# Kernel optimization log

Hardware: AMD Instinct MI355X
Metric: run time of the kernel (lower is better)

The kernel has to match this reference:

```python
import jax, jax.numpy as jnp
import numpy as np

EMBED_DIM = 256
NUM_HEADS = 8
N_Q = 300    # num queries
HW = 4096    # flattened key/value tokens
B = 16       # batch


def _linear(x, W, b):
    # torch nn.Linear: y = x @ W^T + b ; W is [out, in]
    return jnp.einsum('lbc,dc->lbd', x, W) + b


def setup_inputs() -> dict:
    key = jax.random.key(0)
    ks = jax.random.split(key, 32)
    C = EMBED_DIM
    s = 1.0 / np.sqrt(C)
    inp = {
        'query': jax.random.normal(ks[0], (N_Q, B, C), jnp.float32),
        'key': jax.random.normal(ks[1], (HW, B, C), jnp.float32),
        'value': jax.random.normal(ks[2], (HW, B, C), jnp.float32),
        'query_pos': jax.random.normal(ks[3], (N_Q, B, C), jnp.float32),
        'key_pos': jax.random.normal(ks[4], (HW, B, C), jnp.float32),
        'query_sine_embed': jax.random.normal(ks[5], (N_Q, B, C), jnp.float32),
    }
    names = ['qc', 'qp', 'qs', 'kc', 'kp', 'v', 'o']
    for i, nm in enumerate(names):
        inp[f'W_{nm}'] = jax.random.uniform(ks[6 + 2 * i], (C, C), jnp.float32, -s, s)
        inp[f'b_{nm}'] = jax.random.uniform(ks[7 + 2 * i], (C,), jnp.float32, -s, s)
    return inp


def reference(query, key, value, query_pos, key_pos, query_sine_embed,
              W_qc, b_qc, W_qp, b_qp, W_qs, b_qs, W_kc, b_kc,
              W_kp, b_kp, W_v, b_v, W_o, b_o):
    H = NUM_HEADS
    N, Bc, C = query.shape
    L = key.shape[0]
    Dh = C // H
    identity = query

    query_content = _linear(query, W_qc, b_qc)          # [N,B,C]
    key_content = _linear(key, W_kc, b_kc)              # [L,B,C]
    v = _linear(value, W_v, b_v)                        # [L,B,C]
    kp = _linear(key_pos, W_kp, b_kp)                   # [L,B,C]
    # is_first_layer == True branch
    qp = _linear(query_pos, W_qp, b_qp)                 # [N,B,C]
    q = query_content + qp
    k = key_content + kp

    qs = _linear(query_sine_embed, W_qs, b_qs)          # [N,B,C]
    # concat content and positional halves per head -> head dim 2*Dh
    q = jnp.concatenate([q.reshape(N, Bc, H, Dh), qs.reshape(N, Bc, H, Dh)], axis=3)
    k = jnp.concatenate([k.reshape(L, Bc, H, Dh), kp.reshape(L, Bc, H, Dh)], axis=3)

    q = q.transpose(1, 2, 0, 3)                          # [B,H,N,2Dh]
    k = k.transpose(1, 2, 0, 3)                          # [B,H,L,2Dh]
    v = v.reshape(L, Bc, H, Dh).transpose(1, 2, 0, 3)    # [B,H,L,Dh]

    scale = (2 * Dh) ** (-0.5)
    attn = jnp.einsum('bhnd,bhld->bhnl', q * scale, k)   # [B,H,N,L]
    attn = jax.nn.softmax(attn, axis=-1)
    out = jnp.einsum('bhnl,bhld->bhnd', attn, v)         # [B,H,N,Dh]
    out = out.transpose(0, 2, 1, 3).reshape(Bc, N, C)    # [B,N,C]
    out = jnp.einsum('bnc,dc->bnd', out, W_o) + b_o
    out = out.transpose(1, 0, 2)                         # [N,B,C]
    return identity + out
```

## Files before the change

### kernel.cpp

```cpp
#include <hip/hip_runtime.h>
#include <cstdint>
#include <cstddef>


typedef float  f4  __attribute__((ext_vector_type(4)));
typedef __bf16 b8v __attribute__((ext_vector_type(8)));

#define MFMA_BF16(a, b, c) __builtin_amdgcn_mfma_f32_16x16x32_bf16((a), (b), (c), 0, 0, 0)

#define GLD_LDS16(gp, lp)                                             \
  __builtin_amdgcn_global_load_lds(                                   \
      (const __attribute__((address_space(1))) void*)(gp),            \
      (__attribute__((address_space(3))) void*)(lp), 16, 0, 0)

__global__ __launch_bounds__(256) void convert_w(
    const float* __restrict__ W0, const float* __restrict__ W1,
    const float* __restrict__ W2, __bf16* __restrict__ Wbf)
{
  int i = blockIdx.x * 256 + threadIdx.x;
  int base = i * 4;
  int m = base >> 16;
  int off = base & 65535;
  const float* W = (m == 0) ? W0 : (m == 1) ? W1 : W2;
  float4 v = *(const float4*)(W + off);
  __bf16 o[4];
  o[0] = (__bf16)v.x; o[1] = (__bf16)v.y; o[2] = (__bf16)v.z; o[3] = (__bf16)v.w;
  *(uint2*)(Wbf + (size_t)m * 65536 + off) = *(uint2*)o;
}

__global__ __launch_bounds__(256, 2) void key_side_gemm(
    const float* __restrict__ key, const float* __restrict__ key_pos,
    const float* __restrict__ value, const __bf16* __restrict__ Wbf,
    const float* __restrict__ b_kc, const float* __restrict__ b_kp,
    const float* __restrict__ b_v,
    __bf16* __restrict__ K64, __bf16* __restrict__ V32)
{
  __shared__ char smem[65536];
  const int tid  = threadIdx.x;
  const int wave = tid >> 6, lane = tid & 63;
  const int lrow = lane & 15, quad = lane >> 4;
  const int p  = blockIdx.y;
  const int r0 = blockIdx.x * 128;
  const int rowbase = (wave & 1) * 64;
  const int colbase = (wave >> 1) * 128;

  const float* __restrict__ X = (p == 0) ? key : (p == 1) ? key_pos : value;
  const __bf16* __restrict__ Wb = Wbf + (size_t)p * 65536;
  const float* __restrict__ bias = (p == 0) ? b_kc : (p == 1) ? b_kp : b_v;

  auto stageW = [&](int buf, int kc) {
#pragma unroll
    for (int it = 0; it < 8; ++it) {
      int slot = it * 256 + tid;
      int wr = slot >> 3, gp = slot & 7;
      int g  = gp ^ (wr & 7);
      GLD_LDS16(Wb + (size_t)wr * 256 + kc + g * 8, smem + buf * 32768 + slot * 16);
    }
  };
  auto readB = [&](int buf, int ct, int kk4) -> b8v {
    int wr = colbase + ct * 16 + lrow;
    int g  = (kk4 + quad) ^ (wr & 7);
    return *(const b8v*)(smem + buf * 32768 + wr * 128 + g * 16);
  };
  auto loadA = [&](float4* x0, float4* x1, int kc) {
#pragma unroll
    for (int rt = 0; rt < 4; ++rt) {
      const float* xp = X + (size_t)(r0 + rowbase + rt * 16 + lrow) * 256 + kc + quad * 8;
      x0[rt] = *(const float4*)xp;
      x1[rt] = *(const float4*)(xp + 4);
    }
  };
  auto mk = [&](float4 x0, float4 x1) -> b8v {
    b8v t;
    t[0] = (__bf16)x0.x; t[1] = (__bf16)x0.y; t[2] = (__bf16)x0.z; t[3] = (__bf16)x0.w;
    t[4] = (__bf16)x1.x; t[5] = (__bf16)x1.y; t[6] = (__bf16)x1.z; t[7] = (__bf16)x1.w;
    return t;
  };

  f4 acc[4][8];
#pragma unroll
  for (int i = 0; i < 4; ++i)
#pragma unroll
    for (int j = 0; j < 8; ++j) acc[i][j] = f4{0.f, 0.f, 0.f, 0.f};

  float4 c0[4], c1[4], d0[4], d1[4];
  loadA(c0, c1, 0);
  stageW(0, 0);
  __syncthreads();

  for (int s = 0; s < 4; ++s) {
    const int kc0 = s * 64, buf = s & 1;
    loadA(d0, d1, kc0 + 32);
    if (s < 3) stageW(buf ^ 1, kc0 + 64);

    b8v a[4];
#pragma unroll
    for (int rt = 0; rt < 4; ++rt) a[rt] = mk(c0[rt], c1[rt]);
#pragma unroll
    for (int ct = 0; ct < 8; ++ct) {
      b8v bfr = readB(buf, ct, 0);
#pragma unroll
      for (int rt = 0; rt < 4; ++rt) acc[rt][ct] = MFMA_BF16(a[rt], bfr, acc[rt][ct]);
    }

    if (s < 3) loadA(c0, c1, kc0 + 64);

#pragma unroll
    for (int rt = 0; rt < 4; ++rt) a[rt] = mk(d0[rt], d1[rt]);
#pragma unroll
    for (int ct = 0; ct < 8; ++ct) {
      b8v bfr = readB(buf, ct, 4);
#pragma unroll
      for (int rt = 0; rt < 4; ++rt) acc[rt][ct] = MFMA_BF16(a[rt], bfr, acc[rt][ct]);
    }
    __syncthreads();
  }

  __bf16* Os = (__bf16*)smem;
#pragma unroll
  for (int ct = 0; ct < 8; ++ct) {
    int col = colbase + ct * 16 + lrow;
    float bv = bias[col];
#pragma unroll
    for (int rt = 0; rt < 4; ++rt)
#pragma unroll
      for (int r = 0; r < 4; ++r) {
        int row = rowbase + rt * 16 + quad * 4 + r;
        Os[row * 256 + col] = (__bf16)(acc[rt][ct][r] + bv);
      }
  }
  __syncthreads();
#pragma unroll
  for (int it = 0; it < 16; ++it) {
    int chunk = it * 64 + wave * 16 + (lane & 15);
    int q = lane >> 4;
    int row = chunk >> 3, h = chunk & 7;
    int R = r0 + row, l = R >> 4, bb = R & 15;
    uint4 v = *(const uint4*)(Os + chunk * 32 + q * 8);
    __bf16* dst = (p == 2) ? (V32 + ((size_t)(bb * 8 + h) * 4096 + l) * 32)
                           : (K64 + ((size_t)(bb * 8 + h) * 4096 + l) * 64 + p * 32);
    *(uint4*)(dst + q * 8) = v;
  }
}

__global__ __launch_bounds__(256) void query_side_gemm(
    const float* __restrict__ query, const float* __restrict__ query_pos,
    const float* __restrict__ query_sine,
    const float* __restrict__ W_qc, const float* __restrict__ b_qc,
    const float* __restrict__ W_qp, const float* __restrict__ b_qp,
    const float* __restrict__ W_qs, const float* __restrict__ b_qs,
    __bf16* __restrict__ Q64)
{
  __shared__ __bf16 Ws[256][72];
  const int tid  = threadIdx.x;
  const int wave = tid >> 6, lane = tid & 63;
  const int lrow = lane & 15, quad = lane >> 4;
  const int r0 = blockIdx.x * 64;

  f4 acc[16];
#pragma unroll
  for (int i = 0; i < 16; ++i) acc[i] = f4{0.f, 0.f, 0.f, 0.f};

  for (int kc = 0; kc < 768; kc += 64) {
    const float* X; const float* W;
    if (kc < 256)      { X = query;      W = W_qc; }
    else if (kc < 512) { X = query_pos;  W = W_qp; }
    else               { X = query_sine; W = W_qs; }
    const int ko = kc & 255;
#pragma unroll
    for (int it = 0; it < 16; ++it) {
      int idx = it * 256 + tid;
      int row = idx >> 4, c4 = idx & 15;
      float4 w = *(const float4*)(W + (size_t)row * 256 + ko + c4 * 4);
      __bf16* dp = &Ws[row][c4 * 4];
      dp[0] = (__bf16)w.x; dp[1] = (__bf16)w.y; dp[2] = (__bf16)w.z; dp[3] = (__bf16)w.w;
    }
    __syncthreads();
#pragma unroll
    for (int kk = 0; kk < 64; kk += 32) {
      const float* xp = X + (size_t)(r0 + wave * 16 + lrow) * 256 + ko + kk + quad * 8;
      float4 x0 = *(const float4*)xp;
      float4 x1 = *(const float4*)(xp + 4);
      b8v a;
      a[0] = (__bf16)x0.x; a[1] = (__bf16)x0.y; a[2] = (__bf16)x0.z; a[3] = (__bf16)x0.w;
      a[4] = (__bf16)x1.x; a[5] = (__bf16)x1.y; a[6] = (__bf16)x1.z; a[7] = (__bf16)x1.w;
#pragma unroll
      for (int ct = 0; ct < 16; ++ct) {
        b8v bf = *(const b8v*)&Ws[ct * 16 + lrow][kk + quad * 8];
        acc[ct] = MFMA_BF16(a, bf, acc[ct]);
      }
    }
    __syncthreads();
    if (kc == 448) {
#pragma unroll
      for (int ct = 0; ct < 16; ++ct) {
        int col = ct * 16 + lrow;
        float bsum = b_qc[col] + b_qp[col];
        int h = col >> 5, d = col & 31;
#pragma unroll
        for (int r = 0; r < 4; ++r) {
          int row = r0 + wave * 16 + quad * 4 + r;
          int n = row >> 4, bb = row & 15;
          Q64[((size_t)(bb * 8 + h) * 320 + n) * 64 + d] = (__bf16)((acc[ct][r] + bsum) * 0.125f);
        }
      }
    }
  }
#pragma unroll
  for (int ct = 0; ct < 16; ++ct) {
    int col = ct * 16 + lrow;
    float bsum = b_qc[col] + b_qp[col] + b_qs[col];
    int h = col >> 5, d = col & 31;
#pragma unroll
    for (int r = 0; r < 4; ++r) {
      int row = r0 + wave * 16 + quad * 4 + r;
      int n = row >> 4, bb = row & 15;
      Q64[((size_t)(bb * 8 + h) * 320 + n) * 64 + 32 + d] = (__bf16)((acc[ct][r] + bsum) * 0.125f);
    }
  }
}

__global__ __launch_bounds__(256) void attn_kernel(
    const __bf16* __restrict__ Q64, const __bf16* __restrict__ K64,
    const __bf16* __restrict__ V32, __bf16* __restrict__ Obf)
{
  __shared__ __bf16 Ks[128][72];
  __shared__ __bf16 Vt[32][136];
  __shared__ __bf16 Ps[64][136];
  const int tid  = threadIdx.x;
  const int wave = tid >> 6, lane = tid & 63;
  const int lrow = lane & 15, quad = lane >> 4;
  const int bh = blockIdx.y;
  const int n0 = blockIdx.x * 64;

  const __bf16* Qb = Q64 + ((size_t)bh * 320 + n0 + wave * 16 + lrow) * 64;
  const b8v qa0 = *(const b8v*)(Qb + quad * 8);
  const b8v qa1 = *(const b8v*)(Qb + 32 + quad * 8);

  const __bf16* Kb = K64 + (size_t)bh * 4096 * 64;
  const __bf16* Vb = V32 + (size_t)bh * 4096 * 32;

  float mst[4], lst[4];
#pragma unroll
  for (int i = 0; i < 4; ++i) { mst[i] = -1e30f; lst[i] = 0.f; }
  f4 oacc[2];
  oacc[0] = f4{0.f, 0.f, 0.f, 0.f};
  oacc[1] = f4{0.f, 0.f, 0.f, 0.f};

  for (int l0 = 0; l0 < 4096; l0 += 128) {
#pragma unroll
    for (int it = 0; it < 4; ++it) {
      int idx = it * 256 + tid;
      int row = idx >> 3, s = idx & 7;
      *(uint4*)&Ks[row][s * 8] = *(const uint4*)(Kb + (size_t)(l0 + row) * 64 + s * 8);
    }
#pragma unroll
    for (int it = 0; it < 2; ++it) {
      int idx = it * 256 + tid;
      int row = idx >> 2, s = idx & 3;
      uint4 u = *(const uint4*)(Vb + (size_t)(l0 + row) * 32 + s * 8);
      __bf16 tmp[8]; *(uint4*)tmp = u;
      int pc = ((row & 15) << 3) | (row >> 4);
#pragma unroll
      for (int j = 0; j < 8; ++j) Vt[s * 8 + j][pc] = tmp[j];
    }
    __syncthreads();

    f4 sc[8];
#pragma unroll
    for (int ct = 0; ct < 8; ++ct) {
      b8v kb0 = *(const b8v*)&Ks[ct * 16 + lrow][quad * 8];
      b8v kb1 = *(const b8v*)&Ks[ct * 16 + lrow][32 + quad * 8];
      f4 z = f4{0.f, 0.f, 0.f, 0.f};
      z = MFMA_BF16(qa0, kb0, z);
      z = MFMA_BF16(qa1, kb1, z);
      sc[ct] = z;
    }

    float rmax[4], rsum[4], alpha[4];
#pragma unroll
    for (int r = 0; r < 4; ++r) {
      float v = sc[0][r];
#pragma unroll
      for (int ct = 1; ct < 8; ++ct) v = fmaxf(v, sc[ct][r]);
      rmax[r] = v;
    }
#pragma unroll
    for (int off = 8; off >= 1; off >>= 1)
#pragma unroll
      for (int r = 0; r < 4; ++r)
        rmax[r] = fmaxf(rmax[r], __shfl_xor(rmax[r], off, 16));
#pragma unroll
    for (int r = 0; r < 4; ++r) {
      float mnew = fmaxf(mst[r], rmax[r]);
      alpha[r] = __expf(mst[r] - mnew);
      mst[r] = mnew;
    }
#pragma unroll
    for (int ct = 0; ct < 8; ++ct)
#pragma unroll
      for (int r = 0; r < 4; ++r)
        sc[ct][r] = __expf(sc[ct][r] - mst[r]);
#pragma unroll
    for (int r = 0; r < 4; ++r) {
      float v = sc[0][r];
#pragma unroll
      for (int ct = 1; ct < 8; ++ct) v += sc[ct][r];
      rsum[r] = v;
    }
#pragma unroll
    for (int off = 8; off >= 1; off >>= 1)
#pragma unroll
      for (int r = 0; r < 4; ++r)
        rsum[r] += __shfl_xor(rsum[r], off, 16);
#pragma unroll
    for (int r = 0; r < 4; ++r) lst[r] = lst[r] * alpha[r] + rsum[r];
#pragma unroll
    for (int c2 = 0; c2 < 2; ++c2)
#pragma unroll
      for (int r = 0; r < 4; ++r) oacc[c2][r] *= alpha[r];

#pragma unroll
    for (int r = 0; r < 4; ++r) {
      b8v pv;
#pragma unroll
      for (int ct = 0; ct < 8; ++ct) pv[ct] = (__bf16)sc[ct][r];
      *(b8v*)&Ps[wave * 16 + quad * 4 + r][lrow * 8] = pv;
    }

#pragma unroll
    for (int kt = 0; kt < 4; ++kt) {
      b8v pa = *(const b8v*)&Ps[wave * 16 + lrow][kt * 32 + quad * 8];
#pragma unroll
      for (int c2 = 0; c2 < 2; ++c2) {
        b8v vb = *(const b8v*)&Vt[c2 * 16 + lrow][kt * 32 + quad * 8];
        oacc[c2] = MFMA_BF16(pa, vb, oacc[c2]);
      }
    }
    __syncthreads();
  }

  const int bb = bh >> 3, h = bh & 7;
#pragma unroll
  for (int r = 0; r < 4; ++r) {
    int n = n0 + wave * 16 + quad * 4 + r;
    if (n < 300) {
      float inv = 1.0f / lst[r];
#pragma unroll
      for (int c2 = 0; c2 < 2; ++c2) {
        int col = h * 32 + c2 * 16 + lrow;
        Obf[((size_t)bb * 300 + n) * 256 + col] = (__bf16)(oacc[c2][r] * inv);
      }
    }
  }
}

__global__ __launch_bounds__(256) void out_proj_gemm(
    const __bf16* __restrict__ Obf, const float* __restrict__ W_o,
    const float* __restrict__ b_o, const float* __restrict__ query,
    float* __restrict__ out)
{
  __shared__ __bf16 Ws[256][72];
  const int tid  = threadIdx.x;
  const int wave = tid >> 6, lane = tid & 63;
  const int lrow = lane & 15, quad = lane >> 4;
  const int r0 = blockIdx.x * 64;

  f4 acc[16];
#pragma unroll
  for (int i = 0; i < 16; ++i) acc[i] = f4{0.f, 0.f, 0.f, 0.f};

  for (int kc0 = 0; kc0 < 256; kc0 += 64) {
#pragma unroll
    for (int it = 0; it < 16; ++it) {
      int idx = it * 256 + tid;
      int row = idx >> 4, c4 = idx & 15;
      float4 w = *(const float4*)(W_o + (size_t)row * 256 + kc0 + c4 * 4);
      __bf16* dp = &Ws[row][c4 * 4];
      dp[0] = (__bf16)w.x; dp[1] = (__bf16)w.y; dp[2] = (__bf16)w.z; dp[3] = (__bf16)w.w;
    }
    __syncthreads();
#pragma unroll
    for (int kk = 0; kk < 64; kk += 32) {
      b8v a = *(const b8v*)(Obf + (size_t)(r0 + wave * 16 + lrow) * 256 + kc0 + kk + quad * 8);
#pragma unroll
      for (int ct = 0; ct < 16; ++ct) {
        b8v bf = *(const b8v*)&Ws[ct * 16 + lrow][kk + quad * 8];
        acc[ct] = MFMA_BF16(a, bf, acc[ct]);
      }
    }
    __syncthreads();
  }
#pragma unroll
  for (int ct = 0; ct < 16; ++ct) {
    int col = ct * 16 + lrow;
    float bo = b_o[col];
#pragma unroll
    for (int r = 0; r < 4; ++r) {
      int row = r0 + wave * 16 + quad * 4 + r;
      int bb = row / 300, n = row % 300;
      size_t oaddr = ((size_t)n * 16 + bb) * 256 + col;
      out[oaddr] = acc[ct][r] + bo + query[oaddr];
    }
  }
}

extern "C" void kernel_launch(void* const* d_in, const int* in_sizes, int n_in,
                              void* d_out, int out_size, void* d_ws, size_t ws_size,
                              hipStream_t stream) {
  (void)in_sizes; (void)n_in; (void)out_size; (void)ws_size;
  const float* query      = (const float*)d_in[0];
  const float* key        = (const float*)d_in[1];
  const float* value      = (const float*)d_in[2];
  const float* query_pos  = (const float*)d_in[3];
  const float* key_pos    = (const float*)d_in[4];
  const float* query_sine = (const float*)d_in[5];
  const float* W_qc = (const float*)d_in[6];  const float* b_qc = (const float*)d_in[7];
  const float* W_qp = (const float*)d_in[8];  const float* b_qp = (const float*)d_in[9];
  const float* W_qs = (const float*)d_in[10]; const float* b_qs = (const float*)d_in[11];
  const float* W_kc = (const float*)d_in[12]; const float* b_kc = (const float*)d_in[13];
  const float* W_kp = (const float*)d_in[14]; const float* b_kp = (const float*)d_in[15];
  const float* W_v  = (const float*)d_in[16]; const float* b_v  = (const float*)d_in[17];
  const float* W_o  = (const float*)d_in[18]; const float* b_o  = (const float*)d_in[19];
  float* out = (float*)d_out;

  char* ws = (char*)d_ws;
  constexpr size_t K64_BYTES = (size_t)128 * 4096 * 64 * 2;
  constexpr size_t V32_BYTES = (size_t)128 * 4096 * 32 * 2;
  constexpr size_t Q64_BYTES = (size_t)128 * 320 * 64 * 2;
  constexpr size_t OBF_BYTES = (size_t)16 * 300 * 256 * 2;
  __bf16* K64 = (__bf16*)ws;
  __bf16* V32 = (__bf16*)(ws + K64_BYTES);
  __bf16* Q64 = (__bf16*)(ws + K64_BYTES + V32_BYTES);
  __bf16* Obf = (__bf16*)(ws + K64_BYTES + V32_BYTES + Q64_BYTES);
  __bf16* Wbf = (__bf16*)(ws + K64_BYTES + V32_BYTES + Q64_BYTES + OBF_BYTES);

  hipLaunchKernelGGL(convert_w, dim3(192), dim3(256), 0, stream,
                     W_kc, W_kp, W_v, Wbf);
  hipLaunchKernelGGL(key_side_gemm, dim3(512, 3), dim3(256), 0, stream,
                     key, key_pos, value, Wbf, b_kc, b_kp, b_v, K64, V32);
  hipLaunchKernelGGL(query_side_gemm, dim3(75), dim3(256), 0, stream,
                     query, query_pos, query_sine, W_qc, b_qc, W_qp, b_qp, W_qs, b_qs, Q64);
  hipLaunchKernelGGL(attn_kernel, dim3(5, 128), dim3(256), 0, stream,
                     Q64, K64, V32, Obf);
  hipLaunchKernelGGL(out_proj_gemm, dim3(75), dim3(256), 0, stream,
                     Obf, W_o, b_o, query, out);
}
```

Measured before the change: 495.2 us.

## Split attention over key chunks with all queries per block and combine

Restructures attention so each block handles all 320 queries of a head against a quarter of the keys, instead of 64 queries against all keys. Each K/V tile is loaded once per block rather than once per query block. A new combine kernel merges the four partial softmax results using their max and sum statistics. The change also adds register double-buffered K/V prefetch, an XOR-swizzled K layout in LDS, and launch bounds allowing two blocks per CU. The cost is extra partial-output traffic, an additional kernel launch, and much higher register pressure from five query tiles of accumulators per wave.

```diff
diff --git a/kernel.cpp b/kernel.cpp
--- a/kernel.cpp
+++ b/kernel.cpp
@@ -220,139 +220,205 @@
   }
 }
 
-__global__ __launch_bounds__(256) void attn_kernel(
+__global__ __launch_bounds__(256, 2) void attn_part(
     const __bf16* __restrict__ Q64, const __bf16* __restrict__ K64,
-    const __bf16* __restrict__ V32, __bf16* __restrict__ Obf)
+    const __bf16* __restrict__ V32,
+    __bf16* __restrict__ Opart, float* __restrict__ Mpart, float* __restrict__ Lpart)
 {
-  __shared__ __bf16 Ks[128][72];
+  __shared__ __bf16 Ks[128 * 64];
   __shared__ __bf16 Vt[32][136];
-  __shared__ __bf16 Ps[64][136];
+  __shared__ __bf16 Ps[4][16][136];
   const int tid  = threadIdx.x;
   const int wave = tid >> 6, lane = tid & 63;
   const int lrow = lane & 15, quad = lane >> 4;
-  const int bh = blockIdx.y;
-  const int n0 = blockIdx.x * 64;
-
-  const __bf16* Qb = Q64 + ((size_t)bh * 320 + n0 + wave * 16 + lrow) * 64;
-  const b8v qa0 = *(const b8v*)(Qb + quad * 8);
-  const b8v qa1 = *(const b8v*)(Qb + 32 + quad * 8);
+  const int ls = blockIdx.x, bh = blockIdx.y;
+  const int l0base = ls * 1024;
 
   const __bf16* Kb = K64 + (size_t)bh * 4096 * 64;
   const __bf16* Vb = V32 + (size_t)bh * 4096 * 32;
 
-  float mst[4], lst[4];
-#pragma unroll
-  for (int i = 0; i < 4; ++i) { mst[i] = -1e30f; lst[i] = 0.f; }
-  f4 oacc[2];
-  oacc[0] = f4{0.f, 0.f, 0.f, 0.f};
-  oacc[1] = f4{0.f, 0.f, 0.f, 0.f};
-
-  for (int l0 = 0; l0 < 4096; l0 += 128) {
+  b8v qa0[5], qa1[5];
+#pragma unroll
+  for (int t = 0; t < 5; ++t) {
+    const __bf16* Qb = Q64 + ((size_t)bh * 320 + wave * 80 + t * 16 + lrow) * 64;
+    qa0[t] = *(const b8v*)(Qb + quad * 8);
+    qa1[t] = *(const b8v*)(Qb + 32 + quad * 8);
+  }
+
+  const int vk = tid >> 4, vpg = (tid >> 2) & 3, vs = tid & 3;
+  const int vr  = vpg * 32 + vk;
+  const int vpi = vk * 8 + 2 * vpg;
+
+  auto loadKV = [&](uint4* kr, uint4* vv, int c) {
+    int l0 = l0base + c * 128;
 #pragma unroll
     for (int it = 0; it < 4; ++it) {
-      int idx = it * 256 + tid;
-      int row = idx >> 3, s = idx & 7;
-      *(uint4*)&Ks[row][s * 8] = *(const uint4*)(Kb + (size_t)(l0 + row) * 64 + s * 8);
-    }
-#pragma unroll
-    for (int it = 0; it < 2; ++it) {
-      int idx = it * 256 + tid;
-      int row = idx >> 2, s = idx & 3;
-      uint4 u = *(const uint4*)(Vb + (size_t)(l0 + row) * 32 + s * 8);
-      __bf16 tmp[8]; *(uint4*)tmp = u;
-      int pc = ((row & 15) << 3) | (row >> 4);
-#pragma unroll
-      for (int j = 0; j < 8; ++j) Vt[s * 8 + j][pc] = tmp[j];
-    }
-    __syncthreads();
-
-    f4 sc[8];
-#pragma unroll
-    for (int ct = 0; ct < 8; ++ct) {
-      b8v kb0 = *(const b8v*)&Ks[ct * 16 + lrow][quad * 8];
-      b8v kb1 = *(const b8v*)&Ks[ct * 16 + lrow][32 + quad * 8];
-      f4 z = f4{0.f, 0.f, 0.f, 0.f};
-      z = MFMA_BF16(qa0, kb0, z);
-      z = MFMA_BF16(qa1, kb1, z);
-      sc[ct] = z;
-    }
-
-    float rmax[4], rsum[4], alpha[4];
+      int slot = it * 256 + tid, row = slot >> 3, gs = slot & 7;
+      int g = gs ^ (row & 7);
+      kr[it] = *(const uint4*)(Kb + (size_t)(l0 + row) * 64 + g * 8);
+    }
+    vv[0] = *(const uint4*)(Vb + (size_t)(l0 + vr) * 32 + vs * 8);
+    vv[1] = *(const uint4*)(Vb + (size_t)(l0 + vr + 16) * 32 + vs * 8);
+  };
+  auto stage = [&](const uint4* kr, const uint4* vv) {
+#pragma unroll
+    for (int it = 0; it < 4; ++it) {
+      int slot = it * 256 + tid;
+      *(uint4*)((char*)Ks + slot * 16) = kr[it];
+    }
+    __bf16 a[8], b[8];
+    *(uint4*)a = vv[0]; *(uint4*)b = vv[1];
+#pragma unroll
+    for (int j = 0; j < 8; ++j) {
+      __bf16 pr[2] = {a[j], b[j]};
+      *(uint32_t*)&Vt[vs * 8 + j][vpi] = *(const uint32_t*)pr;
+    }
+  };
+  auto readKs = [&](int wr, int g) -> b8v {
+    int gs = g ^ (wr & 7);
+    return *(const b8v*)((const char*)Ks + wr * 128 + gs * 16);
+  };
+
+  float mst[5][4], lst[5][4];
+  f4 oacc[5][2];
+#pragma unroll
+  for (int t = 0; t < 5; ++t) {
+#pragma unroll
+    for (int r = 0; r < 4; ++r) { mst[t][r] = -1e30f; lst[t][r] = 0.f; }
+    oacc[t][0] = f4{0.f, 0.f, 0.f, 0.f};
+    oacc[t][1] = f4{0.f, 0.f, 0.f, 0.f};
+  }
+
+  auto compute = [&]() {
+#pragma unroll
+    for (int t = 0; t < 5; ++t) {
+      f4 sc[8];
+#pragma unroll
+      for (int ct = 0; ct < 8; ++ct) {
+        b8v kb0 = readKs(ct * 16 + lrow, quad);
+        b8v kb1 = readKs(ct * 16 + lrow, 4 + quad);
+        f4 z = f4{0.f, 0.f, 0.f, 0.f};
+        z = MFMA_BF16(qa0[t], kb0, z);
+        z = MFMA_BF16(qa1[t], kb1, z);
+        sc[ct] = z;
+      }
+      float rmax[4], rsum[4], alpha[4];
+#pragma unroll
+      for (int r = 0; r < 4; ++r) {
+        float v = sc[0][r];
+#pragma unroll
+        for (int ct = 1; ct < 8; ++ct) v = fmaxf(v, sc[ct][r]);
+        rmax[r] = v;
+      }
+#pragma unroll
+      for (int off = 8; off >= 1; off >>= 1)
+#pragma unroll
+        for (int r = 0; r < 4; ++r)
+          rmax[r] = fmaxf(rmax[r], __shfl_xor(rmax[r], off, 16));
+#pragma unroll
+      for (int r = 0; r < 4; ++r) {
+        float mnew = fmaxf(mst[t][r], rmax[r]);
+        alpha[r] = __expf(mst[t][r] - mnew);
+        mst[t][r] = mnew;
+      }
+#pragma unroll
+      for (int ct = 0; ct < 8; ++ct)
+#pragma unroll
+        for (int r = 0; r < 4; ++r)
+          sc[ct][r] = __expf(sc[ct][r] - mst[t][r]);
+#pragma unroll
+      for (int r = 0; r < 4; ++r) {
+        float v = sc[0][r];
+#pragma unroll
+        for (int ct = 1; ct < 8; ++ct) v += sc[ct][r];
+        rsum[r] = v;
+      }
+#pragma unroll
+      for (int off = 8; off >= 1; off >>= 1)
+#pragma unroll
+        for (int r = 0; r < 4; ++r)
+          rsum[r] += __shfl_xor(rsum[r], off, 16);
+#pragma unroll
+      for (int r = 0; r < 4; ++r) lst[t][r] = lst[t][r] * alpha[r] + rsum[r];
+#pragma unroll
+      for (int c2 = 0; c2 < 2; ++c2)
+#pragma unroll
+        for (int r = 0; r < 4; ++r) oacc[t][c2][r] *= alpha[r];
+
+#pragma unroll
+      for (int r = 0; r < 4; ++r) {
+        b8v pv;
+#pragma unroll
+        for (int ct = 0; ct < 8; ++ct) pv[ct] = (__bf16)sc[ct][r];
+        *(b8v*)&Ps[wave][quad * 4 + r][lrow * 8] = pv;
+      }
+#pragma unroll
+      for (int kt = 0; kt < 4; ++kt) {
+        b8v pa = *(const b8v*)&Ps[wave][lrow][kt * 32 + quad * 8];
+#pragma unroll
+        for (int c2 = 0; c2 < 2; ++c2) {
+          b8v vb = *(const b8v*)&Vt[c2 * 16 + lrow][kt * 32 + quad * 8];
+          oacc[t][c2] = MFMA_BF16(pa, vb, oacc[t][c2]);
+        }
+      }
+    }
+  };
+
+  uint4 kA[4], vA[2], kB[4], vB[2];
+  loadKV(kA, vA, 0);
+  for (int c = 0; c < 8; c += 2) {
+    __syncthreads();
+    stage(kA, vA);
+    loadKV(kB, vB, c + 1);
+    __syncthreads();
+    compute();
+    __syncthreads();
+    stage(kB, vB);
+    if (c + 2 < 8) loadKV(kA, vA, c + 2);
+    __syncthreads();
+    compute();
+  }
+
+  const size_t pbase = ((size_t)bh * 4 + ls) * 320;
+#pragma unroll
+  for (int t = 0; t < 5; ++t) {
 #pragma unroll
     for (int r = 0; r < 4; ++r) {
-      float v = sc[0][r];
-#pragma unroll
-      for (int ct = 1; ct < 8; ++ct) v = fmaxf(v, sc[ct][r]);
-      rmax[r] = v;
-    }
-#pragma unroll
-    for (int off = 8; off >= 1; off >>= 1)
-#pragma unroll
-      for (int r = 0; r < 4; ++r)
-        rmax[r] = fmaxf(rmax[r], __shfl_xor(rmax[r], off, 16));
-#pragma unroll
-    for (int r = 0; r < 4; ++r) {
-      float mnew = fmaxf(mst[r], rmax[r]);
-      alpha[r] = __expf(mst[r] - mnew);
-      mst[r] = mnew;
-    }
-#pragma unroll
-    for (int ct = 0; ct < 8; ++ct)
-#pragma unroll
-      for (int r = 0; r < 4; ++r)
-        sc[ct][r] = __expf(sc[ct][r] - mst[r]);
-#pragma unroll
-    for (int r = 0; r < 4; ++r) {
-      float v = sc[0][r];
-#pragma unroll
-      for (int ct = 1; ct < 8; ++ct) v += sc[ct][r];
-      rsum[r] = v;
-    }
-#pragma unroll
-    for (int off = 8; off >= 1; off >>= 1)
-#pragma unroll
-      for (int r = 0; r < 4; ++r)
-        rsum[r] += __shfl_xor(rsum[r], off, 16);
-#pragma unroll
-    for (int r = 0; r < 4; ++r) lst[r] = lst[r] * alpha[r] + rsum[r];
-#pragma unroll
-    for (int c2 = 0; c2 < 2; ++c2)
-#pragma unroll
-      for (int r = 0; r < 4; ++r) oacc[c2][r] *= alpha[r];
-
-#pragma unroll
-    for (int r = 0; r < 4; ++r) {
-      b8v pv;
-#pragma unroll
-      for (int ct = 0; ct < 8; ++ct) pv[ct] = (__bf16)sc[ct][r];
-      *(b8v*)&Ps[wave * 16 + quad * 4 + r][lrow * 8] = pv;
-    }
-
-#pragma unroll
-    for (int kt = 0; kt < 4; ++kt) {
-      b8v pa = *(const b8v*)&Ps[wave * 16 + lrow][kt * 32 + quad * 8];
-#pragma unroll
-      for (int c2 = 0; c2 < 2; ++c2) {
-        b8v vb = *(const b8v*)&Vt[c2 * 16 + lrow][kt * 32 + quad * 8];
-        oacc[c2] = MFMA_BF16(pa, vb, oacc[c2]);
-      }
-    }
-    __syncthreads();
-  }
-
-  const int bb = bh >> 3, h = bh & 7;
-#pragma unroll
-  for (int r = 0; r < 4; ++r) {
-    int n = n0 + wave * 16 + quad * 4 + r;
-    if (n < 300) {
-      float inv = 1.0f / lst[r];
-#pragma unroll
-      for (int c2 = 0; c2 < 2; ++c2) {
-        int col = h * 32 + c2 * 16 + lrow;
-        Obf[((size_t)bb * 300 + n) * 256 + col] = (__bf16)(oacc[c2][r] * inv);
-      }
-    }
-  }
+      int q = wave * 80 + t * 16 + quad * 4 + r;
+      float inv = 1.0f / lst[t][r];
+#pragma unroll
+      for (int c2 = 0; c2 < 2; ++c2)
+        Opart[(pbase + q) * 32 + c2 * 16 + lrow] = (__bf16)(oacc[t][c2][r] * inv);
+      if (lrow == 0) {
+        Mpart[pbase + q] = mst[t][r];
+        Lpart[pbase + q] = lst[t][r];
+      }
+    }
+  }
+}
+
+__global__ __launch_bounds__(256) void attn_combine(
+    const __bf16* __restrict__ Opart, const float* __restrict__ Mpart,
+    const float* __restrict__ Lpart, __bf16* __restrict__ Obf)
+{
+  const int bh = blockIdx.y;
+  const int idx = blockIdx.x * 256 + threadIdx.x;
+  const int q = idx >> 5, d = idx & 31;
+  if (q >= 300) return;
+  const size_t rb = ((size_t)bh * 4) * 320 + q;
+  float m0 = Mpart[rb], m1 = Mpart[rb + 320], m2 = Mpart[rb + 640], m3 = Mpart[rb + 960];
+  float M = fmaxf(fmaxf(m0, m1), fmaxf(m2, m3));
+  float w0 = Lpart[rb]       * __expf(m0 - M);
+  float w1 = Lpart[rb + 320] * __expf(m1 - M);
+  float w2 = Lpart[rb + 640] * __expf(m2 - M);
+  float w3 = Lpart[rb + 960] * __expf(m3 - M);
+  float S = w0 + w1 + w2 + w3;
+  float o = w0 * (float)Opart[rb * 32 + d]
+          + w1 * (float)Opart[(rb + 320) * 32 + d]
+          + w2 * (float)Opart[(rb + 640) * 32 + d]
+          + w3 * (float)Opart[(rb + 960) * 32 + d];
+  int b = bh >> 3, h = bh & 7;
+  Obf[((size_t)b * 300 + q) * 256 + h * 32 + d] = (__bf16)(o / S);
 }
 
 __global__ __launch_bounds__(256) void out_proj_gemm(
@@ -429,11 +495,18 @@
   constexpr size_t V32_BYTES = (size_t)128 * 4096 * 32 * 2;
   constexpr size_t Q64_BYTES = (size_t)128 * 320 * 64 * 2;
   constexpr size_t OBF_BYTES = (size_t)16 * 300 * 256 * 2;
+  constexpr size_t WBF_BYTES = (size_t)3 * 256 * 256 * 2;
+  constexpr size_t OPART_BYTES = (size_t)128 * 4 * 320 * 32 * 2;
+  constexpr size_t MPART_BYTES = (size_t)128 * 4 * 320 * 4;
   __bf16* K64 = (__bf16*)ws;
   __bf16* V32 = (__bf16*)(ws + K64_BYTES);
   __bf16* Q64 = (__bf16*)(ws + K64_BYTES + V32_BYTES);
   __bf16* Obf = (__bf16*)(ws + K64_BYTES + V32_BYTES + Q64_BYTES);
   __bf16* Wbf = (__bf16*)(ws + K64_BYTES + V32_BYTES + Q64_BYTES + OBF_BYTES);
+  char*  pbase = ws + K64_BYTES + V32_BYTES + Q64_BYTES + OBF_BYTES + WBF_BYTES;
+  __bf16* Opart = (__bf16*)pbase;
+  float*  Mpart = (float*)(pbase + OPART_BYTES);
+  float*  Lpart = (float*)(pbase + OPART_BYTES + MPART_BYTES);
 
   hipLaunchKernelGGL(convert_w, dim3(192), dim3(256), 0, stream,
                      W_kc, W_kp, W_v, Wbf);
@@ -441,8 +514,10 @@
                      key, key_pos, value, Wbf, b_kc, b_kp, b_v, K64, V32);
   hipLaunchKernelGGL(query_side_gemm, dim3(75), dim3(256), 0, stream,
                      query, query_pos, query_sine, W_qc, b_qc, W_qp, b_qp, W_qs, b_qs, Q64);
-  hipLaunchKernelGGL(attn_kernel, dim3(5, 128), dim3(256), 0, stream,
-                     Q64, K64, V32, Obf);
+  hipLaunchKernelGGL(attn_part, dim3(4, 128), dim3(256), 0, stream,
+                     Q64, K64, V32, Opart, Mpart, Lpart);
+  hipLaunchKernelGGL(attn_combine, dim3(40, 128), dim3(256), 0, stream,
+                     Opart, Mpart, Lpart, Obf);
   hipLaunchKernelGGL(out_proj_gemm, dim3(75), dim3(256), 0, stream,
                      Obf, W_o, b_o, query, out);
 }
```

After: 514.8 us. 1.04x slower.
